# Kernel optimization log

Hardware: AMD Instinct MI355X
Metric: run time of the kernel (lower is better)

Reference implementation:

```python
import jax, jax.numpy as jnp
import numpy as np

B, P, H, N, D, K = 1024, 1024, 4096, 32, 512, 128


def setup_inputs() -> dict:
    key = jax.random.key(0)
    k1, k2, k3, k4, k5 = jax.random.split(key, 5)
    return {
        "proximal_input": jax.random.normal(k1, (B, P), dtype=jnp.float32),
        "distal_input": jax.random.normal(k2, (B, D), dtype=jnp.float32),
        "W": jax.random.normal(k3, (H, P), dtype=jnp.float32) / np.sqrt(P),
        "b": jax.random.normal(k4, (H,), dtype=jnp.float32) / np.sqrt(P),
        "distal": jax.random.normal(k5, (H, N, D), dtype=jnp.float32),
        "k": K,
    }


def reference(proximal_input, distal_input, W, b, distal, k):
    # proximal path: standard linear -> (B, H)
    proximal_output = proximal_input @ W.T + b
    # per-hidden-unit dendrite projections -> (H, B, N)
    distal_output = jnp.einsum('bd,hnd->hbn', distal_input, distal)
    # pick dominant dendrite by absolute value, keep its signed value
    abs_max_idx = jnp.argmax(jnp.abs(distal_output), axis=-1)          # (H, B)
    distal_max = jnp.take_along_axis(
        distal_output, abs_max_idx[..., None], axis=-1)[..., 0].T      # (B, H)
    # sigmoid gate modulates proximal activations
    result = proximal_output * jax.nn.sigmoid(distal_max)              # (B, H)
    # keep only top-k per row (scatter-built 0/1 mask, as in the original)
    _, top_idxs = jax.lax.top_k(result, k)                             # (B, k)
    rows = jnp.arange(result.shape[0])[:, None]
    mask = jnp.zeros_like(result).at[rows, top_idxs].set(1.0)
    return result * mask
```

## Files before the change

kernel.cpp:

```cpp
#include <hip/hip_runtime.h>
#include <cstdint>
#include <cmath>

#define Bsz  1024
#define Pdim 1024
#define Hdim 4096
#define Ndim 32
#define Ddim 512
#define Ktop 128

typedef _Float16 f16x8  __attribute__((ext_vector_type(8)));
typedef float    f32x16 __attribute__((ext_vector_type(16)));

#define GLDS(gsrc, ldst)                                                        \
  __builtin_amdgcn_global_load_lds(                                             \
      (const __attribute__((address_space(1))) unsigned int*)(gsrc),            \
      (__attribute__((address_space(3))) unsigned int*)(ldst), 16, 0, 0)

#define WS_NEEDED 270532608ull

__global__ __launch_bounds__(256) void convert_img(
    const float* __restrict__ src, char* __restrict__ dst, int kcbits)
{
  const int gid  = blockIdx.x * 256 + threadIdx.x;
  const int row  = gid >> kcbits;
  const int e    = (gid & ((1 << kcbits) - 1)) * 8;
  const int Krow = 8 << kcbits;
  float4 v0 = *(const float4*)(src + (size_t)row * Krow + e);
  float4 v1 = *(const float4*)(src + (size_t)row * Krow + e + 4);
  const int tile = row >> 7, r = row & 127, ks = e >> 5, k = e & 31;
  char* base = dst + (size_t)(tile * (Krow >> 5) + ks) * 16384;
  const int off = ((r >> 5) * 2 + (k >> 4)) * 1024
                + ((r & 31) + 32 * ((k >> 3) & 1)) * 16;
  const float f[8] = {v0.x, v0.y, v0.z, v0.w, v1.x, v1.y, v1.z, v1.w};
  f16x8 hi, lo;
#pragma unroll
  for (int j = 0; j < 8; j++) {
    const _Float16 h = (_Float16)f[j];
    hi[j] = h;
    lo[j] = (_Float16)((f[j] - (float)h) * 256.f);
  }
  *(f16x8*)(base + off)        = hi;
  *(f16x8*)(base + 8192 + off) = lo;
}

#define PIPE_LOOP(NH)                                                           \
  STAGE(0);                                                                     \
  STAGE(1);                                                                     \
  for (int h = 0; h < (NH); ++h) {                                              \
    if (h + 2 < (NH)) {                                                         \
      STAGE(h + 2);                                                             \
      asm volatile("s_waitcnt vmcnt(8)" ::: "memory");                          \
    } else if (h + 1 < (NH)) {                                                  \
      asm volatile("s_waitcnt vmcnt(4)" ::: "memory");                          \
    } else {                                                                    \
      asm volatile("s_waitcnt vmcnt(0)" ::: "memory");                          \
    }                                                                           \
    __builtin_amdgcn_s_barrier();                                               \
    asm volatile("" ::: "memory");                                              \
    const char* buf = lds[h & 3];                                               \
    f16x8 ah[2], al[2], bh[2], bl[2];                                           \
    _Pragma("unroll")                                                           \
    for (int mi = 0; mi < 2; mi++) {                                            \
      const int m = wr * 2 + mi;                                                \
      ah[mi] = *(const f16x8*)(buf + m * 1024 + lane16);                        \
      al[mi] = *(const f16x8*)(buf + 4096 + m * 1024 + lane16);                 \
    }                                                                           \
    _Pragma("unroll")                                                           \
    for (int ni = 0; ni < 2; ni++) {                                            \
      const int m = wc * 2 + ni;                                                \
      bh[ni] = *(const f16x8*)(buf + 8192 + m * 1024 + lane16);                 \
      bl[ni] = *(const f16x8*)(buf + 12288 + m * 1024 + lane16);                \
    }                                                                           \
    __builtin_amdgcn_s_setprio(1);                                              \
    _Pragma("unroll")                                                           \
    for (int ni = 0; ni < 2; ni++)                                              \
      _Pragma("unroll")                                                         \
      for (int mi = 0; mi < 2; mi++) {                                          \
        acc[mi][ni]  = __builtin_amdgcn_mfma_f32_32x32x16_f16(ah[mi], bh[ni], acc[mi][ni],  0, 0, 0); \
        accx[mi][ni] = __builtin_amdgcn_mfma_f32_32x32x16_f16(ah[mi], bl[ni], accx[mi][ni], 0, 0, 0); \
        accx[mi][ni] = __builtin_amdgcn_mfma_f32_32x32x16_f16(al[mi], bh[ni], accx[mi][ni], 0, 0, 0); \
      }                                                                         \
    __builtin_amdgcn_s_setprio(0);                                              \
  }

__global__ __launch_bounds__(256, 2) void proximal_mfma(
    const char* __restrict__ Aw, const char* __restrict__ Bw,
    const float* __restrict__ bias, float* __restrict__ out)
{
  __shared__ __align__(16) char lds[4][16384];
  const int t = threadIdx.x, lane = t & 63, wv = t >> 6;
  const int lane16 = lane * 16;
  const int hi32 = lane >> 5, c31 = lane & 31;
  const int wr = wv >> 1, wc = wv & 1;

  const int blk = blockIdx.x;
  const int xcd = blk & 7, q = blk >> 3;
  const int htile = xcd * 4 + (q >> 3);
  const int btile = q & 7;
  const int h0 = htile * 128, b0 = btile * 128;
  if (q & 1) __builtin_amdgcn_s_sleep(7);

  f32x16 acc[2][2], accx[2][2];
#pragma unroll
  for (int mi = 0; mi < 2; mi++)
#pragma unroll
    for (int ni = 0; ni < 2; ni++) {
      acc[mi][ni]  = (f32x16)(0.f);
      accx[mi][ni] = (f32x16)(0.f);
    }

  const char* Abase = Aw + (size_t)(htile * 32) * 16384;
  const char* Bbase = Bw + (size_t)(btile * 32) * 16384;

  auto STAGE = [&](int h) {
    const int ks = h >> 1, kk = h & 1;
    char* buf = lds[h & 3];
    const char* Ai = Abase + (size_t)ks * 16384;
    const char* Bi = Bbase + (size_t)ks * 16384;
    const char* srcs[4] = {Ai, Ai + 8192, Bi, Bi + 8192};
#pragma unroll
    for (int j = 0; j < 4; j++) {
      const int c = j * 4 + wv;
      GLDS(srcs[j] + (wv * 2 + kk) * 1024 + lane16, buf + c * 1024);
    }
  };

  PIPE_LOOP(64)

#pragma unroll
  for (int mi = 0; mi < 2; ++mi)
#pragma unroll
    for (int ni = 0; ni < 2; ++ni) {
      const int bcol = b0 + wc * 64 + ni * 32 + c31;
#pragma unroll
      for (int qq = 0; qq < 4; ++qq) {
        const int hb = h0 + wr * 64 + mi * 32 + qq * 8 + hi32 * 4;
        const float4 bb = *(const float4*)(bias + hb);
        float4 o;
        o.x = acc[mi][ni][4*qq+0] + accx[mi][ni][4*qq+0] * 0.00390625f + bb.x;
        o.y = acc[mi][ni][4*qq+1] + accx[mi][ni][4*qq+1] * 0.00390625f + bb.y;
        o.z = acc[mi][ni][4*qq+2] + accx[mi][ni][4*qq+2] * 0.00390625f + bb.z;
        o.w = acc[mi][ni][4*qq+3] + accx[mi][ni][4*qq+3] * 0.00390625f + bb.w;
        *(float4*)(out + (size_t)bcol * Hdim + hb) = o;
      }
    }
}

__global__ __launch_bounds__(256, 2) void distal_mfma(
    const char* __restrict__ Aw, const char* __restrict__ Bw,
    float* __restrict__ out)
{
  __shared__ __align__(16) char lds[4][16384];
  const int t = threadIdx.x, lane = t & 63, wv = t >> 6;
  const int lane16 = lane * 16;
  const int hi32 = lane >> 5, c31 = lane & 31;
  const int wr = wv >> 1, wc = wv & 1;

  const int blk = blockIdx.x;
  const int xcd = blk & 7, q = blk >> 3;
  const int ntile = xcd * 128 + (q >> 3);
  const int btile = q & 7;
  if (q & 1) __builtin_amdgcn_s_sleep(7);

  f32x16 acc[2][2], accx[2][2];
#pragma unroll
  for (int mi = 0; mi < 2; mi++)
#pragma unroll
    for (int ni = 0; ni < 2; ni++) {
      acc[mi][ni]  = (f32x16)(0.f);
      accx[mi][ni] = (f32x16)(0.f);
    }

  const char* Abase = Aw + (size_t)(ntile * 16) * 16384;
  const char* Bbase = Bw + (size_t)(btile * 16) * 16384;

  auto STAGE = [&](int h) {
    const int ks = h >> 1, kk = h & 1;
    char* buf = lds[h & 3];
    const char* Ai = Abase + (size_t)ks * 16384;
    const char* Bi = Bbase + (size_t)ks * 16384;
    const char* srcs[4] = {Ai, Ai + 8192, Bi, Bi + 8192};
#pragma unroll
    for (int j = 0; j < 4; j++) {
      const int c = j * 4 + wv;
      GLDS(srcs[j] + (wv * 2 + kk) * 1024 + lane16, buf + c * 1024);
    }
  };

  PIPE_LOOP(32)

#pragma unroll
  for (int mi = 0; mi < 2; ++mi)
#pragma unroll
    for (int ni = 0; ni < 2; ++ni) {
      float bestA = -1.f, bestV = 0.f;
      int   bestN = 999;
#pragma unroll
      for (int reg = 0; reg < 16; ++reg) {
        const float v = acc[mi][ni][reg] + accx[mi][ni][reg] * 0.00390625f;
        const float a = fabsf(v);
        const int   n = (reg & 3) + 8 * (reg >> 2) + 4 * hi32;
        if (a > bestA) { bestA = a; bestV = v; bestN = n; }
      }
      {
        const float oa = __shfl_xor(bestA, 32, 64);
        const float ov = __shfl_xor(bestV, 32, 64);
        const int   on = __shfl_xor(bestN, 32, 64);
        if (oa > bestA || (oa == bestA && on < bestN)) {
          bestA = oa; bestV = ov; bestN = on;
        }
      }
      if (hi32 == 0) {
        const int bcol = btile * 128 + wc * 64 + ni * 32 + c31;
        const int h    = ntile * 4 + wr * 2 + mi;
        const float gate = 1.f / (1.f + expf(-bestV));
        out[(size_t)bcol * Hdim + h] *= gate;
      }
    }
}

__global__ __launch_bounds__(256) void proximal_gemm(
    const float* __restrict__ pin, const float* __restrict__ W,
    const float* __restrict__ bias, float* __restrict__ out)
{
  __shared__ float Blds[32 * 256];
  __shared__ float Alds[32 * 32];
  const int t  = threadIdx.x;
  const int l  = t & 63;
  const int wv = t >> 6;
  const int ell   = blockIdx.x;
  const int xcd   = ell & 7;
  const int q     = ell >> 3;
  const int htile = xcd * 2 + (q >> 5);
  const int btile = q & 31;
  const int h0 = htile * 256, b0 = btile * 32;

  float acc[8][4];
#pragma unroll
  for (int i = 0; i < 8; i++)
    for (int j = 0; j < 4; j++) acc[i][j] = 0.f;

  const float* wrow = W + (size_t)(h0 + t) * Pdim;
  const int ab = t >> 3, ak = (t & 7) * 4;
  const float* arow = pin + (size_t)(b0 + ab) * Pdim + ak;

  for (int kt = 0; kt < Pdim / 32; ++kt) {
    const int p0 = kt * 32;
    float wbuf[32];
#pragma unroll
    for (int f = 0; f < 8; f++) {
      float4 v = *(const float4*)(wrow + p0 + f * 4);
      wbuf[f * 4 + 0] = v.x; wbuf[f * 4 + 1] = v.y;
      wbuf[f * 4 + 2] = v.z; wbuf[f * 4 + 3] = v.w;
    }
    float4 av = *(const float4*)(arow + p0);
    __syncthreads();
#pragma unroll
    for (int f = 0; f < 32; f++) Blds[f * 256 + t] = wbuf[f];
    Alds[(ak + 0) * 32 + ab] = av.x;
    Alds[(ak + 1) * 32 + ab] = av.y;
    Alds[(ak + 2) * 32 + ab] = av.z;
    Alds[(ak + 3) * 32 + ab] = av.w;
    __syncthreads();
#pragma unroll
    for (int k = 0; k < 32; k++) {
      float4 bv  = *(const float4*)&Blds[k * 256 + 4 * l];
      float4 alo = *(const float4*)&Alds[k * 32 + 8 * wv];
      float4 ahi = *(const float4*)&Alds[k * 32 + 8 * wv + 4];
      float a0[8] = {alo.x, alo.y, alo.z, alo.w, ahi.x, ahi.y, ahi.z, ahi.w};
#pragma unroll
      for (int i = 0; i < 8; i++) {
        acc[i][0] += a0[i] * bv.x;
        acc[i][1] += a0[i] * bv.y;
        acc[i][2] += a0[i] * bv.z;
        acc[i][3] += a0[i] * bv.w;
      }
    }
  }
  float4 bb = *(const float4*)(bias + h0 + 4 * l);
#pragma unroll
  for (int i = 0; i < 8; i++) {
    float4 o;
    o.x = acc[i][0] + bb.x;
    o.y = acc[i][1] + bb.y;
    o.z = acc[i][2] + bb.z;
    o.w = acc[i][3] + bb.w;
    *(float4*)(out + (size_t)(b0 + 8 * wv + i) * Hdim + h0 + 4 * l) = o;
  }
}

__global__ __launch_bounds__(256) void distal_gate_fb(
    const float* __restrict__ din, const float* __restrict__ distal,
    float* __restrict__ out)
{
  __shared__ float Blds[32 * 256];
  __shared__ float Alds[32 * 32];
  const int t  = threadIdx.x;
  const int l  = t & 63;
  const int wv = t >> 6;
  const int ell   = blockIdx.x;
  const int xcd   = ell & 7;
  const int q     = ell >> 3;
  const int htile = xcd * 64 + (q >> 5);
  const int btile = q & 31;
  const int n0 = htile * 256, b0 = btile * 32;

  float acc[8][4];
#pragma unroll
  for (int i = 0; i < 8; i++)
    for (int j = 0; j < 4; j++) acc[i][j] = 0.f;

  const float* brow = distal + (size_t)(n0 + t) * Ddim;
  const int ab = t >> 3, ak = (t & 7) * 4;
  const float* arow = din + (size_t)(b0 + ab) * Ddim + ak;

  for (int kt = 0; kt < Ddim / 32; ++kt) {
    const int d0 = kt * 32;
    float wbuf[32];
#pragma unroll
    for (int f = 0; f < 8; f++) {
      float4 v = *(const float4*)(brow + d0 + f * 4);
      wbuf[f * 4 + 0] = v.x; wbuf[f * 4 + 1] = v.y;
      wbuf[f * 4 + 2] = v.z; wbuf[f * 4 + 3] = v.w;
    }
    float4 av = *(const float4*)(arow + d0);
    __syncthreads();
#pragma unroll
    for (int f = 0; f < 32; f++) Blds[f * 256 + t] = wbuf[f];
    Alds[(ak + 0) * 32 + ab] = av.x;
    Alds[(ak + 1) * 32 + ab] = av.y;
    Alds[(ak + 2) * 32 + ab] = av.z;
    Alds[(ak + 3) * 32 + ab] = av.w;
    __syncthreads();
#pragma unroll
    for (int k = 0; k < 32; k++) {
      float4 bv  = *(const float4*)&Blds[k * 256 + 4 * l];
      float4 alo = *(const float4*)&Alds[k * 32 + 8 * wv];
      float4 ahi = *(const float4*)&Alds[k * 32 + 8 * wv + 4];
      float a0[8] = {alo.x, alo.y, alo.z, alo.w, ahi.x, ahi.y, ahi.z, ahi.w};
#pragma unroll
      for (int i = 0; i < 8; i++) {
        acc[i][0] += a0[i] * bv.x;
        acc[i][1] += a0[i] * bv.y;
        acc[i][2] += a0[i] * bv.z;
        acc[i][3] += a0[i] * bv.w;
      }
    }
  }
  const int i0  = l & 7;
  const int grp = l >> 3;
  float v = 0.f;
#pragma unroll
  for (int bi = 0; bi < 8; bi++) {
    float bav = fabsf(acc[bi][0]);
    float bv_ = acc[bi][0];
    int   bn  = 4 * i0;
#pragma unroll
    for (int j = 1; j < 4; j++) {
      float av2 = fabsf(acc[bi][j]);
      if (av2 > bav) { bav = av2; bv_ = acc[bi][j]; bn = 4 * i0 + j; }
    }
#pragma unroll
    for (int m = 1; m < 8; m <<= 1) {
      float oav = __shfl_xor(bav, m, 64);
      float ov  = __shfl_xor(bv_, m, 64);
      int   on  = __shfl_xor(bn,  m, 64);
      if (oav > bav || (oav == bav && on < bn)) { bav = oav; bv_ = ov; bn = on; }
    }
    if (bi == i0) v = bv_;
  }
  const float gate = 1.f / (1.f + expf(-v));
  const size_t idx = (size_t)(b0 + 8 * wv + i0) * Hdim + (size_t)htile * 8 + grp;
  out[idx] *= gate;
}

__device__ __forceinline__ unsigned keyf(float f) {
  unsigned u = __float_as_uint(f);
  return (u & 0x80000000u) ? ~u : (u | 0x80000000u);
}

__global__ __launch_bounds__(256) void topk_mask(float* __restrict__ out)
{
  __shared__ float vals[Hdim];
  __shared__ unsigned hist[256];
  __shared__ unsigned sc[4];
  __shared__ unsigned s_prefix, s_kk;
  const int t = threadIdx.x;
  float* row = out + (size_t)blockIdx.x * Hdim;

#pragma unroll
  for (int qq = 0; qq < 4; qq++) {
    float4 v = *(const float4*)(row + qq * 1024 + t * 4);
    *(float4*)&vals[qq * 1024 + t * 4] = v;
  }
  if (t == 0) { s_prefix = 0u; s_kk = Ktop; }
  __syncthreads();

  for (int shift = 24; shift >= 0; shift -= 8) {
    hist[t] = 0u;
    __syncthreads();
    const unsigned prefix = s_prefix;
    const unsigned maskhi = (shift == 24) ? 0u : (0xFFFFFFFFu << (shift + 8));
    for (int c = 0; c < 16; c++) {
      unsigned u = keyf(vals[c * 256 + t]);
      if ((u & maskhi) == prefix)
        atomicAdd(&hist[(u >> shift) & 255u], 1u);
    }
    __syncthreads();
    if (t == 0) {
      unsigned kk = s_kk, cum = 0;
      int bin = 255;
      for (; bin > 0; --bin) {
        unsigned c = hist[bin];
        if (cum + c >= kk) break;
        cum += c;
      }
      s_kk = kk - cum;
      s_prefix = prefix | ((unsigned)bin << shift);
    }
    __syncthreads();
  }
  const unsigned T  = s_prefix;
  const unsigned kk = s_kk;

  const int lane = t & 63, w = t >> 6;
  unsigned running = 0;
  for (int c = 0; c < 16; c++) {
    const int h = c * 256 + t;
    const float v = vals[h];
    const unsigned u = keyf(v);
    const bool tie = (u == T);
    unsigned long long m = __ballot(tie);
    unsigned lpfx = (unsigned)__popcll(m & ((1ull << lane) - 1ull));
    if (lane == 0) sc[w] = (unsigned)__popcll(m);
    __syncthreads();
    unsigned off = 0;
#pragma unroll
    for (int ww = 0; ww < 4; ww++) if (ww < w) off += sc[ww];
    const unsigned rank = running + off + lpfx;
    row[h] = (u > T) ? v : ((tie && rank < kk) ? v : 0.f);
    const unsigned tot = sc[0] + sc[1] + sc[2] + sc[3];
    __syncthreads();
    running += tot;
  }
}

extern "C" void kernel_launch(void* const* d_in, const int* in_sizes, int n_in,
                              void* d_out, int out_size, void* d_ws, size_t ws_size,
                              hipStream_t stream)
{
  (void)in_sizes; (void)n_in; (void)out_size;
  const float* pin  = (const float*)d_in[0];
  const float* dinp = (const float*)d_in[1];
  const float* W    = (const float*)d_in[2];
  const float* bias = (const float*)d_in[3];
  const float* dst  = (const float*)d_in[4];
  float* out = (float*)d_out;

  if (ws_size >= WS_NEEDED) {
    char* ws = (char*)d_ws;
    hipLaunchKernelGGL(convert_img,   dim3(2048),  dim3(256), 0, stream, W,   ws,             7);
    hipLaunchKernelGGL(convert_img,   dim3(512),   dim3(256), 0, stream, pin, ws + 16777216,  7);
    hipLaunchKernelGGL(proximal_mfma, dim3(256),   dim3(256), 0, stream, ws, ws + 16777216, bias, out);
    hipLaunchKernelGGL(convert_img,   dim3(32768), dim3(256), 0, stream, dst,  ws,             6);
    hipLaunchKernelGGL(convert_img,   dim3(256),   dim3(256), 0, stream, dinp, ws + 268435456, 6);
    hipLaunchKernelGGL(distal_mfma,   dim3(8192),  dim3(256), 0, stream, ws, ws + 268435456, out);
  } else {
    hipLaunchKernelGGL(proximal_gemm, dim3(512),   dim3(256), 0, stream, pin, W, bias, out);
    hipLaunchKernelGGL(distal_gate_fb, dim3(16384), dim3(256), 0, stream, dinp, dst, out);
  }

  hipLaunchKernelGGL(topk_mask, dim3(Bsz), dim3(256), 0, stream, out);
}
```

Before: 617.4 us.

## Fuse proximal and distal MFMA GEMMs into one launch and restructure pipeline

Merges the proximal and distal GEMMs into a single kernel whose first 256 blocks do the proximal GEMM and the rest the distal GEMM. Gates go to a separate workspace buffer and are applied in the top-k kernel, so the two paths no longer have to run in order. The shared pipeline also changes its schedule: LDS fragments are loaded before the next stage is issued, with one barrier per iteration and sched_barriers. It drops the s_sleep staggering and needs a larger workspace, plus an extra gate buffer read and write.

```diff
diff --git a/kernel.cpp b/kernel.cpp
--- a/kernel.cpp
+++ b/kernel.cpp
@@ -17,7 +17,12 @@
       (const __attribute__((address_space(1))) unsigned int*)(gsrc),            \
       (__attribute__((address_space(3))) unsigned int*)(ldst), 16, 0, 0)
 
-#define WS_NEEDED 270532608ull
+#define WS_SERIAL 270532608ull
+#define OFF_DIN   268435456ull
+#define OFF_W     270532608ull
+#define OFF_PIN   287309824ull
+#define OFF_GATE  291504128ull
+#define WS_FUSED  308281344ull
 
 __global__ __launch_bounds__(256) void convert_img(
     const float* __restrict__ src, char* __restrict__ dst, int kcbits)
@@ -44,75 +49,12 @@
   *(f16x8*)(base + 8192 + off) = lo;
 }
 
-#define PIPE_LOOP(NH)                                                           \
-  STAGE(0);                                                                     \
-  STAGE(1);                                                                     \
-  for (int h = 0; h < (NH); ++h) {                                              \
-    if (h + 2 < (NH)) {                                                         \
-      STAGE(h + 2);                                                             \
-      asm volatile("s_waitcnt vmcnt(8)" ::: "memory");                          \
-    } else if (h + 1 < (NH)) {                                                  \
-      asm volatile("s_waitcnt vmcnt(4)" ::: "memory");                          \
-    } else {                                                                    \
-      asm volatile("s_waitcnt vmcnt(0)" ::: "memory");                          \
-    }                                                                           \
-    __builtin_amdgcn_s_barrier();                                               \
-    asm volatile("" ::: "memory");                                              \
-    const char* buf = lds[h & 3];                                               \
-    f16x8 ah[2], al[2], bh[2], bl[2];                                           \
-    _Pragma("unroll")                                                           \
-    for (int mi = 0; mi < 2; mi++) {                                            \
-      const int m = wr * 2 + mi;                                                \
-      ah[mi] = *(const f16x8*)(buf + m * 1024 + lane16);                        \
-      al[mi] = *(const f16x8*)(buf + 4096 + m * 1024 + lane16);                 \
-    }                                                                           \
-    _Pragma("unroll")                                                           \
-    for (int ni = 0; ni < 2; ni++) {                                            \
-      const int m = wc * 2 + ni;                                                \
-      bh[ni] = *(const f16x8*)(buf + 8192 + m * 1024 + lane16);                 \
-      bl[ni] = *(const f16x8*)(buf + 12288 + m * 1024 + lane16);                \
-    }                                                                           \
-    __builtin_amdgcn_s_setprio(1);                                              \
-    _Pragma("unroll")                                                           \
-    for (int ni = 0; ni < 2; ni++)                                              \
-      _Pragma("unroll")                                                         \
-      for (int mi = 0; mi < 2; mi++) {                                          \
-        acc[mi][ni]  = __builtin_amdgcn_mfma_f32_32x32x16_f16(ah[mi], bh[ni], acc[mi][ni],  0, 0, 0); \
-        accx[mi][ni] = __builtin_amdgcn_mfma_f32_32x32x16_f16(ah[mi], bl[ni], accx[mi][ni], 0, 0, 0); \
-        accx[mi][ni] = __builtin_amdgcn_mfma_f32_32x32x16_f16(al[mi], bh[ni], accx[mi][ni], 0, 0, 0); \
-      }                                                                         \
-    __builtin_amdgcn_s_setprio(0);                                              \
-  }
-
-__global__ __launch_bounds__(256, 2) void proximal_mfma(
-    const char* __restrict__ Aw, const char* __restrict__ Bw,
-    const float* __restrict__ bias, float* __restrict__ out)
-{
-  __shared__ __align__(16) char lds[4][16384];
-  const int t = threadIdx.x, lane = t & 63, wv = t >> 6;
-  const int lane16 = lane * 16;
-  const int hi32 = lane >> 5, c31 = lane & 31;
-  const int wr = wv >> 1, wc = wv & 1;
-
-  const int blk = blockIdx.x;
-  const int xcd = blk & 7, q = blk >> 3;
-  const int htile = xcd * 4 + (q >> 3);
-  const int btile = q & 7;
-  const int h0 = htile * 128, b0 = btile * 128;
-  if (q & 1) __builtin_amdgcn_s_sleep(7);
-
-  f32x16 acc[2][2], accx[2][2];
-#pragma unroll
-  for (int mi = 0; mi < 2; mi++)
-#pragma unroll
-    for (int ni = 0; ni < 2; ni++) {
-      acc[mi][ni]  = (f32x16)(0.f);
-      accx[mi][ni] = (f32x16)(0.f);
-    }
-
-  const char* Abase = Aw + (size_t)(htile * 32) * 16384;
-  const char* Bbase = Bw + (size_t)(btile * 32) * 16384;
-
+template <int NH>
+__device__ __forceinline__ void pipe_gemm(
+    char (*lds)[16384], const char* Abase, const char* Bbase,
+    int lane16, int wv, int wr, int wc,
+    f32x16 acc[2][2], f32x16 accx[2][2])
+{
   auto STAGE = [&](int h) {
     const int ks = h >> 1, kk = h & 1;
     char* buf = lds[h & 3];
@@ -126,8 +68,57 @@
     }
   };
 
-  PIPE_LOOP(64)
-
+  STAGE(0);
+  STAGE(1);
+  asm volatile("s_waitcnt vmcnt(4)" ::: "memory");
+  __builtin_amdgcn_s_barrier();
+  __builtin_amdgcn_sched_barrier(0);
+
+  for (int h = 0; h < NH; ++h) {
+    const char* buf = lds[h & 3];
+    f16x8 ah[2], al[2], bh[2], bl[2];
+#pragma unroll
+    for (int mi = 0; mi < 2; mi++) {
+      const int m = wr * 2 + mi;
+      ah[mi] = *(const f16x8*)(buf + m * 1024 + lane16);
+      al[mi] = *(const f16x8*)(buf + 4096 + m * 1024 + lane16);
+    }
+#pragma unroll
+    for (int ni = 0; ni < 2; ni++) {
+      const int m = wc * 2 + ni;
+      bh[ni] = *(const f16x8*)(buf + 8192 + m * 1024 + lane16);
+      bl[ni] = *(const f16x8*)(buf + 12288 + m * 1024 + lane16);
+    }
+    __builtin_amdgcn_sched_barrier(0);
+    if (h + 2 < NH) STAGE(h + 2);
+    __builtin_amdgcn_s_barrier();
+    __builtin_amdgcn_sched_barrier(0);
+    __builtin_amdgcn_s_setprio(1);
+#pragma unroll
+    for (int ni = 0; ni < 2; ni++)
+#pragma unroll
+      for (int mi = 0; mi < 2; mi++) {
+        acc[mi][ni]  = __builtin_amdgcn_mfma_f32_32x32x16_f16(ah[mi], bh[ni], acc[mi][ni],  0, 0, 0);
+        accx[mi][ni] = __builtin_amdgcn_mfma_f32_32x32x16_f16(ah[mi], bl[ni], accx[mi][ni], 0, 0, 0);
+        accx[mi][ni] = __builtin_amdgcn_mfma_f32_32x32x16_f16(al[mi], bh[ni], accx[mi][ni], 0, 0, 0);
+      }
+    __builtin_amdgcn_s_setprio(0);
+    if (h + 2 < NH) {
+      asm volatile("s_waitcnt vmcnt(4)" ::: "memory");
+    } else if (h + 1 < NH) {
+      asm volatile("s_waitcnt vmcnt(0)" ::: "memory");
+    }
+    if (h + 1 < NH) {
+      __builtin_amdgcn_s_barrier();
+      __builtin_amdgcn_sched_barrier(0);
+    }
+  }
+}
+
+__device__ __forceinline__ void epi_prox(
+    f32x16 acc[2][2], f32x16 accx[2][2], const float* bias, float* out,
+    int h0, int b0, int wr, int wc, int hi32, int c31)
+{
 #pragma unroll
   for (int mi = 0; mi < 2; ++mi)
 #pragma unroll
@@ -147,49 +138,10 @@
     }
 }
 
-__global__ __launch_bounds__(256, 2) void distal_mfma(
-    const char* __restrict__ Aw, const char* __restrict__ Bw,
-    float* __restrict__ out)
-{
-  __shared__ __align__(16) char lds[4][16384];
-  const int t = threadIdx.x, lane = t & 63, wv = t >> 6;
-  const int lane16 = lane * 16;
-  const int hi32 = lane >> 5, c31 = lane & 31;
-  const int wr = wv >> 1, wc = wv & 1;
-
-  const int blk = blockIdx.x;
-  const int xcd = blk & 7, q = blk >> 3;
-  const int ntile = xcd * 128 + (q >> 3);
-  const int btile = q & 7;
-  if (q & 1) __builtin_amdgcn_s_sleep(7);
-
-  f32x16 acc[2][2], accx[2][2];
-#pragma unroll
-  for (int mi = 0; mi < 2; mi++)
-#pragma unroll
-    for (int ni = 0; ni < 2; ni++) {
-      acc[mi][ni]  = (f32x16)(0.f);
-      accx[mi][ni] = (f32x16)(0.f);
-    }
-
-  const char* Abase = Aw + (size_t)(ntile * 16) * 16384;
-  const char* Bbase = Bw + (size_t)(btile * 16) * 16384;
-
-  auto STAGE = [&](int h) {
-    const int ks = h >> 1, kk = h & 1;
-    char* buf = lds[h & 3];
-    const char* Ai = Abase + (size_t)ks * 16384;
-    const char* Bi = Bbase + (size_t)ks * 16384;
-    const char* srcs[4] = {Ai, Ai + 8192, Bi, Bi + 8192};
-#pragma unroll
-    for (int j = 0; j < 4; j++) {
-      const int c = j * 4 + wv;
-      GLDS(srcs[j] + (wv * 2 + kk) * 1024 + lane16, buf + c * 1024);
-    }
-  };
-
-  PIPE_LOOP(32)
-
+__device__ __forceinline__ void epi_distal(
+    f32x16 acc[2][2], f32x16 accx[2][2], float* out, float* gates,
+    int ntile, int btile, int wr, int wc, int hi32, int c31)
+{
 #pragma unroll
   for (int mi = 0; mi < 2; ++mi)
 #pragma unroll
@@ -215,9 +167,109 @@
         const int bcol = btile * 128 + wc * 64 + ni * 32 + c31;
         const int h    = ntile * 4 + wr * 2 + mi;
         const float gate = 1.f / (1.f + expf(-bestV));
-        out[(size_t)bcol * Hdim + h] *= gate;
-      }
-    }
+        const size_t idx = (size_t)bcol * Hdim + h;
+        if (gates) gates[idx] = gate;
+        else       out[idx] *= gate;
+      }
+    }
+}
+
+__global__ __launch_bounds__(256, 2) void fused_mfma(
+    const char* __restrict__ Wimg, const char* __restrict__ Pimg,
+    const float* __restrict__ bias, float* __restrict__ out,
+    const char* __restrict__ Dimg, const char* __restrict__ Nimg,
+    float* __restrict__ gates)
+{
+  __shared__ __align__(16) char lds[4][16384];
+  const int t = threadIdx.x, lane = t & 63, wv = t >> 6;
+  const int lane16 = lane * 16;
+  const int hi32 = lane >> 5, c31 = lane & 31;
+  const int wr = wv >> 1, wc = wv & 1;
+
+  f32x16 acc[2][2], accx[2][2];
+#pragma unroll
+  for (int mi = 0; mi < 2; mi++)
+#pragma unroll
+    for (int ni = 0; ni < 2; ni++) {
+      acc[mi][ni]  = (f32x16)(0.f);
+      accx[mi][ni] = (f32x16)(0.f);
+    }
+
+  if (blockIdx.x < 256) {
+    const int blk = blockIdx.x;
+    const int xcd = blk & 7, q = blk >> 3;
+    const int htile = xcd * 4 + (q >> 3);
+    const int btile = q & 7;
+    pipe_gemm<64>(lds, Wimg + (size_t)(htile * 32) * 16384,
+                  Pimg + (size_t)(btile * 32) * 16384,
+                  lane16, wv, wr, wc, acc, accx);
+    epi_prox(acc, accx, bias, out, htile * 128, btile * 128, wr, wc, hi32, c31);
+  } else {
+    const int blk = blockIdx.x - 256;
+    const int xcd = blk & 7, q = blk >> 3;
+    const int ntile = xcd * 128 + (q >> 3);
+    const int btile = q & 7;
+    pipe_gemm<32>(lds, Dimg + (size_t)(ntile * 16) * 16384,
+                  Nimg + (size_t)(btile * 16) * 16384,
+                  lane16, wv, wr, wc, acc, accx);
+    epi_distal(acc, accx, out, gates, ntile, btile, wr, wc, hi32, c31);
+  }
+}
+
+__global__ __launch_bounds__(256, 2) void proximal_mfma(
+    const char* __restrict__ Aw, const char* __restrict__ Bw,
+    const float* __restrict__ bias, float* __restrict__ out)
+{
+  __shared__ __align__(16) char lds[4][16384];
+  const int t = threadIdx.x, lane = t & 63, wv = t >> 6;
+  const int lane16 = lane * 16;
+  const int hi32 = lane >> 5, c31 = lane & 31;
+  const int wr = wv >> 1, wc = wv & 1;
+  const int blk = blockIdx.x;
+  const int xcd = blk & 7, q = blk >> 3;
+  const int htile = xcd * 4 + (q >> 3);
+  const int btile = q & 7;
+
+  f32x16 acc[2][2], accx[2][2];
+#pragma unroll
+  for (int mi = 0; mi < 2; mi++)
+#pragma unroll
+    for (int ni = 0; ni < 2; ni++) {
+      acc[mi][ni]  = (f32x16)(0.f);
+      accx[mi][ni] = (f32x16)(0.f);
+    }
+  pipe_gemm<64>(lds, Aw + (size_t)(htile * 32) * 16384,
+                Bw + (size_t)(btile * 32) * 16384,
+                lane16, wv, wr, wc, acc, accx);
+  epi_prox(acc, accx, bias, out, htile * 128, btile * 128, wr, wc, hi32, c31);
+}
+
+__global__ __launch_bounds__(256, 2) void distal_mfma(
+    const char* __restrict__ Aw, const char* __restrict__ Bw,
+    float* __restrict__ out)
+{
+  __shared__ __align__(16) char lds[4][16384];
+  const int t = threadIdx.x, lane = t & 63, wv = t >> 6;
+  const int lane16 = lane * 16;
+  const int hi32 = lane >> 5, c31 = lane & 31;
+  const int wr = wv >> 1, wc = wv & 1;
+  const int blk = blockIdx.x;
+  const int xcd = blk & 7, q = blk >> 3;
+  const int ntile = xcd * 128 + (q >> 3);
+  const int btile = q & 7;
+
+  f32x16 acc[2][2], accx[2][2];
+#pragma unroll
+  for (int mi = 0; mi < 2; mi++)
+#pragma unroll
+    for (int ni = 0; ni < 2; ni++) {
+      acc[mi][ni]  = (f32x16)(0.f);
+      accx[mi][ni] = (f32x16)(0.f);
+    }
+  pipe_gemm<32>(lds, Aw + (size_t)(ntile * 16) * 16384,
+                Bw + (size_t)(btile * 16) * 16384,
+                lane16, wv, wr, wc, acc, accx);
+  epi_distal(acc, accx, out, nullptr, ntile, btile, wr, wc, hi32, c31);
 }
 
 __global__ __launch_bounds__(256) void proximal_gemm(
@@ -380,7 +432,8 @@
   return (u & 0x80000000u) ? ~u : (u | 0x80000000u);
 }
 
-__global__ __launch_bounds__(256) void topk_mask(float* __restrict__ out)
+__global__ __launch_bounds__(256) void topk_mask(
+    float* __restrict__ out, const float* __restrict__ gates)
 {
   __shared__ float vals[Hdim];
   __shared__ unsigned hist[256];
@@ -388,10 +441,15 @@
   __shared__ unsigned s_prefix, s_kk;
   const int t = threadIdx.x;
   float* row = out + (size_t)blockIdx.x * Hdim;
+  const float* grow = gates ? gates + (size_t)blockIdx.x * Hdim : nullptr;
 
 #pragma unroll
   for (int qq = 0; qq < 4; qq++) {
     float4 v = *(const float4*)(row + qq * 1024 + t * 4);
+    if (grow) {
+      float4 g = *(const float4*)(grow + qq * 1024 + t * 4);
+      v.x *= g.x; v.y *= g.y; v.z *= g.z; v.w *= g.w;
+    }
     *(float4*)&vals[qq * 1024 + t * 4] = v;
   }
   if (t == 0) { s_prefix = 0u; s_kk = Ktop; }
@@ -458,18 +516,28 @@
   const float* dst  = (const float*)d_in[4];
   float* out = (float*)d_out;
 
-  if (ws_size >= WS_NEEDED) {
-    char* ws = (char*)d_ws;
-    hipLaunchKernelGGL(convert_img,   dim3(2048),  dim3(256), 0, stream, W,   ws,             7);
-    hipLaunchKernelGGL(convert_img,   dim3(512),   dim3(256), 0, stream, pin, ws + 16777216,  7);
+  char* ws = (char*)d_ws;
+  if (ws_size >= WS_FUSED) {
+    hipLaunchKernelGGL(convert_img, dim3(32768), dim3(256), 0, stream, dst,  ws,            6);
+    hipLaunchKernelGGL(convert_img, dim3(256),   dim3(256), 0, stream, dinp, ws + OFF_DIN,  6);
+    hipLaunchKernelGGL(convert_img, dim3(2048),  dim3(256), 0, stream, W,    ws + OFF_W,    7);
+    hipLaunchKernelGGL(convert_img, dim3(512),   dim3(256), 0, stream, pin,  ws + OFF_PIN,  7);
+    hipLaunchKernelGGL(fused_mfma,  dim3(8448),  dim3(256), 0, stream,
+                       ws + OFF_W, ws + OFF_PIN, bias, out,
+                       ws, ws + OFF_DIN, (float*)(ws + OFF_GATE));
+    hipLaunchKernelGGL(topk_mask,   dim3(Bsz),   dim3(256), 0, stream, out,
+                       (const float*)(ws + OFF_GATE));
+  } else if (ws_size >= WS_SERIAL) {
+    hipLaunchKernelGGL(convert_img,   dim3(2048),  dim3(256), 0, stream, W,   ws,            7);
+    hipLaunchKernelGGL(convert_img,   dim3(512),   dim3(256), 0, stream, pin, ws + 16777216, 7);
     hipLaunchKernelGGL(proximal_mfma, dim3(256),   dim3(256), 0, stream, ws, ws + 16777216, bias, out);
-    hipLaunchKernelGGL(convert_img,   dim3(32768), dim3(256), 0, stream, dst,  ws,             6);
-    hipLaunchKernelGGL(convert_img,   dim3(256),   dim3(256), 0, stream, dinp, ws + 268435456, 6);
-    hipLaunchKernelGGL(distal_mfma,   dim3(8192),  dim3(256), 0, stream, ws, ws + 268435456, out);
+    hipLaunchKernelGGL(convert_img,   dim3(32768), dim3(256), 0, stream, dst,  ws,           6);
+    hipLaunchKernelGGL(convert_img,   dim3(256),   dim3(256), 0, stream, dinp, ws + OFF_DIN, 6);
+    hipLaunchKernelGGL(distal_mfma,   dim3(8192),  dim3(256), 0, stream, ws, ws + OFF_DIN, out);
+    hipLaunchKernelGGL(topk_mask,     dim3(Bsz),   dim3(256), 0, stream, out, (const float*)nullptr);
   } else {
-    hipLaunchKernelGGL(proximal_gemm, dim3(512),   dim3(256), 0, stream, pin, W, bias, out);
+    hipLaunchKernelGGL(proximal_gemm,  dim3(512),   dim3(256), 0, stream, pin, W, bias, out);
     hipLaunchKernelGGL(distal_gate_fb, dim3(16384), dim3(256), 0, stream, dinp, dst, out);
-  }
-
-  hipLaunchKernelGGL(topk_mask, dim3(Bsz), dim3(256), 0, stream, out);
-}
+    hipLaunchKernelGGL(topk_mask,      dim3(Bsz),   dim3(256), 0, stream, out, (const float*)nullptr);
+  }
+}
```

After: 601.7 us. 2.5% less time.
